# Performance work log

Measured on AMD Instinct MI355X. Metric: run time of the kernel, lower is better.

The kernel has to match this reference:

```python
import jax, jax.numpy as jnp
import numpy as np

N_NODES = 100000
N_EDGES = 1600000
N_ADJS = 2
N_LAYERS = 3
D_IN = 128
H = 128           # hidden dim; last conv out = 256 / num_adjs = 128
N_GRAPHS = 1024


def setup_inputs() -> dict:
    key = jax.random.key(0)
    ks = jax.random.split(key, 12)
    x = jax.random.normal(ks[0], (N_NODES, D_IN), dtype=jnp.float32)
    edge_index = jax.random.randint(ks[1], (N_ADJS, 2, N_EDGES), 0, N_NODES, dtype=jnp.int32)
    batch = jnp.sort(jax.random.randint(ks[2], (N_NODES,), 0, N_GRAPHS, dtype=jnp.int32))
    s = 0.05
    lin0_w = jax.random.normal(ks[3], (D_IN, H), dtype=jnp.float32) * s
    lin0_b = jnp.zeros((H,), dtype=jnp.float32)
    conv_w = jax.random.normal(ks[4], (N_ADJS, N_LAYERS, H, H), dtype=jnp.float32) * s
    lin1_w = jax.random.normal(ks[5], (2 * H, H), dtype=jnp.float32) * s
    lin1_b = jnp.zeros((H,), dtype=jnp.float32)
    lin2_w = jax.random.normal(ks[6], (H, 1), dtype=jnp.float32) * s
    lin2_b = jnp.zeros((1,), dtype=jnp.float32)
    return {"x": x, "edge_index": edge_index, "batch": batch,
            "lin0_w": lin0_w, "lin0_b": lin0_b, "conv_w": conv_w,
            "lin1_w": lin1_w, "lin1_b": lin1_b, "lin2_w": lin2_w, "lin2_b": lin2_b}


def _gcn_conv(h, W, row, col, norm, n_nodes):
    # GCNConv (bias=False): out[i] = sum_{j->i} norm_e * (h @ W)[j]
    m = h @ W                                  # [N, H] dense transform first (PyG order)
    msg = m[row] * norm[:, None]               # [E+N, H] gather + edge scaling
    return jax.ops.segment_sum(msg, col, num_segments=n_nodes)


def reference(x, edge_index, batch, lin0_w, lin0_b, conv_w, lin1_w, lin1_b, lin2_w, lin2_b):
    n = x.shape[0]
    loops = jnp.arange(n, dtype=edge_index.dtype)
    x0 = jax.nn.relu(x @ lin0_w + lin0_b)      # lin0 + relu
    pooled = []
    for a in range(N_ADJS):
        # gcn_norm with self loops: deg over targets, norm = d^-1/2[row] * d^-1/2[col]
        row = jnp.concatenate([edge_index[a, 0], loops])
        col = jnp.concatenate([edge_index[a, 1], loops])
        deg = jax.ops.segment_sum(jnp.ones_like(col, dtype=x.dtype), col, num_segments=n)
        dis = jnp.where(deg > 0, jax.lax.rsqrt(jnp.maximum(deg, 1e-12)), 0.0)
        norm = dis[row] * dis[col]
        h = x0
        for l in range(N_LAYERS):
            h = jax.nn.relu(_gcn_conv(h, conv_w[a, l], row, col, norm, n))
        # global_add_pool: segment sum over graph ids
        pooled.append(jax.ops.segment_sum(h, batch, num_segments=N_GRAPHS))
    g = jnp.concatenate(pooled, axis=1)        # [G, 256]
    g = jax.nn.relu(g @ lin1_w + lin1_b)
    # dropout(p=0.5) is identity in eval mode
    return g @ lin2_w + lin2_b                 # [G, 1]
```

## Files before the change

kernel.cpp:

```cpp
#include <hip/hip_runtime.h>

#define NN 100000
#define NE 1600000
#define NADJ 2
#define NLAY 3
#define HD 128
#define NG 1024

#define EBLK 4096
#define EB   391
#define NBUK 196
#define BPAD 200
#define GB   782
#define AB   12500
#define PB   1563

typedef unsigned int uint32;
typedef unsigned short u16;

typedef __attribute__((ext_vector_type(8))) short bfrag8;
typedef __attribute__((ext_vector_type(4))) float f32x4;
typedef __attribute__((ext_vector_type(2))) float f32x2;

__device__ __forceinline__ u16 f2bf(float f) {
    uint32 u = __float_as_uint(f);
    u += 0x7FFFu + ((u >> 16) & 1u);
    return (u16)(u >> 16);
}
__device__ __forceinline__ float bflo(uint32 u) { return __uint_as_float(u << 16); }
__device__ __forceinline__ float bfhi(uint32 u) { return __uint_as_float(u & 0xFFFF0000u); }

__global__ __launch_bounds__(256) void prep(
    const float* __restrict__ x, const float* __restrict__ conv_w,
    const float* __restrict__ lin0_w, u16* __restrict__ xbf,
    u16* __restrict__ wt) {
    if (blockIdx.x < 6250) {
        int i = blockIdx.x * 256 + threadIdx.x;
        float4 a = ((const float4*)x)[i * 2];
        float4 b = ((const float4*)x)[i * 2 + 1];
        uint4 v;
        v.x = (uint32)f2bf(a.x) | ((uint32)f2bf(a.y) << 16);
        v.y = (uint32)f2bf(a.z) | ((uint32)f2bf(a.w) << 16);
        v.z = (uint32)f2bf(b.x) | ((uint32)f2bf(b.y) << 16);
        v.w = (uint32)f2bf(b.z) | ((uint32)f2bf(b.w) << 16);
        ((uint4*)xbf)[i] = v;
    } else {
        int bid = blockIdx.x - 6250;
        const float* W = (bid < 6) ? conv_w + (size_t)bid * HD * HD : lin0_w;
        u16* o = wt + (size_t)bid * HD * HD;
        for (int i = 0; i < 64; ++i) {
            int idx = i * 256 + threadIdx.x;
            int n = idx >> 7, k = idx & 127;
            o[idx] = f2bf(W[k * 128 + n]);
        }
    }
}

__global__ __launch_bounds__(256) void gemm_mfma(
    const u16* __restrict__ Abf, const u16* __restrict__ Wt,
    u16* __restrict__ outbf, const float* __restrict__ bias)
{
    const int wid = blockIdx.x * 4 + (threadIdx.x >> 6);
    const int lane = threadIdx.x & 63;
    const int row0 = (wid >> 1) * 64;
    if (row0 >= NN) return;
    const int wc = (wid & 1) * 64;
    const int lr = lane & 15, kg = lane >> 4;

    bfrag8 a[4][4];
    #pragma unroll
    for (int ks = 0; ks < 4; ++ks)
        #pragma unroll
        for (int i = 0; i < 4; ++i)
            a[ks][i] = *(const bfrag8*)&Wt[(size_t)(wc + i * 16 + lr) * 128
                                           + (ks * 4 + kg) * 8];

    const f32x4 z = {0.f, 0.f, 0.f, 0.f};
    f32x4 acc[4][4];
    #pragma unroll
    for (int j = 0; j < 4; ++j)
        #pragma unroll
        for (int i = 0; i < 4; ++i) acc[j][i] = z;

    #pragma unroll
    for (int ks = 0; ks < 4; ++ks) {
        bfrag8 b[4];
        #pragma unroll
        for (int j = 0; j < 4; ++j) {
            int r = min(row0 + j * 16 + lr, NN - 1);
            b[j] = *(const bfrag8*)&Abf[(size_t)r * 128 + (ks * 4 + kg) * 8];
        }
        #pragma unroll
        for (int j = 0; j < 4; ++j)
            #pragma unroll
            for (int i = 0; i < 4; ++i)
                acc[j][i] = __builtin_amdgcn_mfma_f32_16x16x32_bf16(
                    a[ks][i], b[j], acc[j][i], 0, 0, 0);
    }

    #pragma unroll
    for (int j = 0; j < 4; ++j) {
        int m = row0 + j * 16 + lr;
        if (m < NN) {
            #pragma unroll
            for (int i = 0; i < 4; ++i) {
                int colb = wc + i * 16 + kg * 4;
                float4 bb = *(const float4*)&bias[colb];
                float v0 = fmaxf(acc[j][i][0] + bb.x, 0.f);
                float v1 = fmaxf(acc[j][i][1] + bb.y, 0.f);
                float v2 = fmaxf(acc[j][i][2] + bb.z, 0.f);
                float v3 = fmaxf(acc[j][i][3] + bb.w, 0.f);
                uint2 pk;
                pk.x = (uint32)f2bf(v0) | ((uint32)f2bf(v1) << 16);
                pk.y = (uint32)f2bf(v2) | ((uint32)f2bf(v3) << 16);
                *(uint2*)&outbf[(size_t)m * 128 + colb] = pk;
            }
        }
    }
}

__global__ __launch_bounds__(256) void gemm_mfma_b(
    const u16* __restrict__ hbase, int shared, const u16* __restrict__ wt,
    int l, u16* __restrict__ mm2, const float* __restrict__ dis2)
{
    int aa = blockIdx.x >= GB ? 1 : 0;
    int bblk = blockIdx.x - aa * GB;
    const u16* Abf = shared ? hbase : hbase + (size_t)aa * NN * HD;
    const u16* Wt = wt + (size_t)(aa * NLAY + l) * HD * HD;
    u16* outbf = mm2 + (size_t)aa * NN * HD;
    const float* dis = dis2 + (size_t)aa * NN;

    const int wid = bblk * 4 + (threadIdx.x >> 6);
    const int lane = threadIdx.x & 63;
    const int row0 = (wid >> 1) * 64;
    if (row0 >= NN) return;
    const int wc = (wid & 1) * 64;
    const int lr = lane & 15, kg = lane >> 4;

    bfrag8 a[4][4];
    #pragma unroll
    for (int ks = 0; ks < 4; ++ks)
        #pragma unroll
        for (int i = 0; i < 4; ++i)
            a[ks][i] = *(const bfrag8*)&Wt[(size_t)(wc + i * 16 + lr) * 128
                                           + (ks * 4 + kg) * 8];

    const f32x4 z = {0.f, 0.f, 0.f, 0.f};
    f32x4 acc[4][4];
    #pragma unroll
    for (int j = 0; j < 4; ++j)
        #pragma unroll
        for (int i = 0; i < 4; ++i) acc[j][i] = z;

    #pragma unroll
    for (int ks = 0; ks < 4; ++ks) {
        bfrag8 b[4];
        #pragma unroll
        for (int j = 0; j < 4; ++j) {
            int r = min(row0 + j * 16 + lr, NN - 1);
            b[j] = *(const bfrag8*)&Abf[(size_t)r * 128 + (ks * 4 + kg) * 8];
        }
        #pragma unroll
        for (int j = 0; j < 4; ++j)
            #pragma unroll
            for (int i = 0; i < 4; ++i)
                acc[j][i] = __builtin_amdgcn_mfma_f32_16x16x32_bf16(
                    a[ks][i], b[j], acc[j][i], 0, 0, 0);
    }

    #pragma unroll
    for (int j = 0; j < 4; ++j) {
        int m = row0 + j * 16 + lr;
        if (m < NN) {
            float ds = dis[m];
            #pragma unroll
            for (int i = 0; i < 4; ++i) {
                int colb = wc + i * 16 + kg * 4;
                uint2 pk;
                pk.x = (uint32)f2bf(acc[j][i][0] * ds)
                     | ((uint32)f2bf(acc[j][i][1] * ds) << 16);
                pk.y = (uint32)f2bf(acc[j][i][2] * ds)
                     | ((uint32)f2bf(acc[j][i][3] * ds) << 16);
                *(uint2*)&outbf[(size_t)m * 128 + colb] = pk;
            }
        }
    }
}


__global__ __launch_bounds__(256) void p1_count(
    const int* __restrict__ ei, int* __restrict__ bcnt)
{
    __shared__ int h[NBUK];
    int aa = blockIdx.x >= EB ? 1 : 0;
    int blk = blockIdx.x - aa * EB;
    const int* col = ei + (size_t)aa * 2 * NE + NE;
    int* bc = bcnt + (size_t)aa * EB * BPAD;
    int t = threadIdx.x;
    if (t < NBUK) h[t] = 0;
    __syncthreads();
    int base = blk * EBLK + t;
    #pragma unroll
    for (int u = 0; u < 16; ++u) {
        int e = base + u * 256;
        if (e < NE) atomicAdd(&h[col[e] >> 9], 1);
    }
    __syncthreads();
    if (t < NBUK) bc[blk * BPAD + t] = h[t];
}

__global__ __launch_bounds__(256) void p2a_scanblocks(
    const int* __restrict__ bcnt, int* __restrict__ pscan,
    int* __restrict__ btot)
{
    __shared__ int s[256];
    int aa = blockIdx.x >= NBUK ? 1 : 0;
    int b = blockIdx.x - aa * NBUK;
    const int* bc = bcnt + (size_t)aa * EB * BPAD;
    int* ps = pscan + (size_t)aa * EB * BPAD;
    int* bt = btot + aa * BPAD;
    int t = threadIdx.x;
    int v[2];
    int loc = 0;
    #pragma unroll
    for (int j = 0; j < 2; ++j) {
        int idx = t * 2 + j;
        v[j] = (idx < EB) ? bc[idx * BPAD + b] : 0;
        loc += v[j];
    }
    s[t] = loc;
    __syncthreads();
    for (int off = 1; off < 256; off <<= 1) {
        int u = (t >= off) ? s[t - off] : 0;
        __syncthreads();
        s[t] += u;
        __syncthreads();
    }
    int pre = s[t] - loc;
    #pragma unroll
    for (int j = 0; j < 2; ++j) {
        int idx = t * 2 + j;
        if (idx < EB) ps[idx * BPAD + b] = pre;
        pre += v[j];
    }
    if (t == 255) bt[b] = s[255];
}

__global__ __launch_bounds__(256) void p2b_scanbuckets(
    const int* __restrict__ btot, int* __restrict__ bbase)
{
    __shared__ int s[256];
    int aa = blockIdx.x;
    const int* bt = btot + aa * BPAD;
    int* bb = bbase + aa * (NBUK + 1);
    int t = threadIdx.x;
    int v = (t < NBUK) ? bt[t] : 0;
    s[t] = v;
    __syncthreads();
    for (int off = 1; off < 256; off <<= 1) {
        int u = (t >= off) ? s[t - off] : 0;
        __syncthreads();
        s[t] += u;
        __syncthreads();
    }
    if (t < NBUK) bb[t] = s[t] - v;
    if (t == NBUK - 1) bb[NBUK] = s[t];
}

__global__ __launch_bounds__(256) void p3_partition(
    const int* __restrict__ ei, const int* __restrict__ pscan,
    const int* __restrict__ bbase, uint2* __restrict__ part)
{
    __shared__ int spre[NBUK];
    __shared__ int cur[NBUK];
    int aa = blockIdx.x >= EB ? 1 : 0;
    int blk = blockIdx.x - aa * EB;
    const int* row = ei + (size_t)aa * 2 * NE;
    const int* col = row + NE;
    const int* ps = pscan + (size_t)aa * EB * BPAD;
    const int* bb = bbase + aa * (NBUK + 1);
    uint2* pt = part + (size_t)aa * NE;
    int t = threadIdx.x;
    if (t < NBUK) {
        spre[t] = bb[t] + ps[blk * BPAD + t];
        cur[t] = 0;
    }
    __syncthreads();
    int base = blk * EBLK + t;
    #pragma unroll
    for (int u = 0; u < 16; ++u) {
        int e = base + u * 256;
        if (e < NE) {
            int c = col[e];
            int b = c >> 9;
            int rk = atomicAdd(&cur[b], 1);
            pt[spre[b] + rk] = make_uint2((uint32)row[e], (uint32)c);
        }
    }
}

__global__ __launch_bounds__(256) void p4_csr(
    const uint2* __restrict__ part, const int* __restrict__ bbase,
    int* __restrict__ row_ptr2, float* __restrict__ dis2,
    int* __restrict__ csr2)
{
    __shared__ int cnt[512];
    __shared__ int sexcl[512];
    __shared__ int cur[512];
    __shared__ int s[256];
    int aa = blockIdx.x >= NBUK ? 1 : 0;
    int b = blockIdx.x - aa * NBUK;
    const uint2* pt = part + (size_t)aa * NE;
    const int* bb = bbase + aa * (NBUK + 1);
    int* rp = row_ptr2 + (size_t)aa * (NN + 1);
    float* ds = dis2 + (size_t)aa * NN;
    int* cs = csr2 + (size_t)aa * NE;
    int t = threadIdx.x;
    int base = bb[b];
    int ecnt = bb[b + 1] - base;
    int n0 = b << 9;
    cnt[t] = 0; cnt[t + 256] = 0;
    cur[t] = 0; cur[t + 256] = 0;
    __syncthreads();
    for (int i = t; i < ecnt; i += 256)
        atomicAdd(&cnt[pt[base + i].y - n0], 1);
    __syncthreads();
    int c0 = cnt[2 * t], c1 = cnt[2 * t + 1];
    int loc = c0 + c1;
    s[t] = loc;
    __syncthreads();
    for (int off = 1; off < 256; off <<= 1) {
        int u = (t >= off) ? s[t - off] : 0;
        __syncthreads();
        s[t] += u;
        __syncthreads();
    }
    int pre = s[t] - loc;
    sexcl[2 * t] = pre;
    sexcl[2 * t + 1] = pre + c0;
    int node = n0 + 2 * t;
    if (node < NN) {
        rp[node] = base + pre;
        ds[node] = rsqrtf((float)(c0 + 1));
    }
    if (node + 1 < NN) {
        rp[node + 1] = base + pre + c0;
        ds[node + 1] = rsqrtf((float)(c1 + 1));
    }
    if (b == 0 && t == 0) rp[NN] = NE;
    __syncthreads();
    for (int i = t; i < ecnt; i += 256) {
        uint2 p = pt[base + i];
        int li = (int)p.y - n0;
        int rk = atomicAdd(&cur[li], 1);
        cs[base + sexcl[li] + rk] = (int)p.x;
    }
}

__global__ __launch_bounds__(256) void agg_relu_b(
    const u16* __restrict__ mm2, const int* __restrict__ row_ptr2,
    const int* __restrict__ csr2, const float* __restrict__ dis2,
    u16* __restrict__ h2)
{
    int aa = blockIdx.x >= AB ? 1 : 0;
    int blk = blockIdx.x - aa * AB;
    const u16* mm = mm2 + (size_t)aa * NN * HD;
    const int* row_ptr = row_ptr2 + (size_t)aa * (NN + 1);
    const int* csr_src = csr2 + (size_t)aa * NE;
    const float* dis = dis2 + (size_t)aa * NN;
    u16* out = h2 + (size_t)aa * NN * HD;

    int wid = blk * 4 + (threadIdx.x >> 6);
    int nodeA = wid * 2;
    if (nodeA >= NN) return;
    int nodeB = nodeA + 1;
    uint32 lane = threadIdx.x & 63;
    const uint32* mv = (const uint32*)mm;
    int lan16 = (int)(lane & 15);

    uint32 selfA = mv[(uint32)nodeA * 64u + lane];
    uint32 selfB = mv[(uint32)nodeB * 64u + lane];
    f32x2 accA, accB;
    accA.x = bflo(selfA); accA.y = bfhi(selfA);
    accB.x = bflo(selfB); accB.y = bfhi(selfB);
    int eA = row_ptr[nodeA], e1A = row_ptr[nodeA + 1];
    int eB = e1A,            e1B = row_ptr[nodeB + 1];

    while (eA + 16 <= e1A && eB + 16 <= e1B) {
        uint32 pA = (uint32)csr_src[eA + lan16];
        uint32 pB = (uint32)csr_src[eB + lan16];
        #pragma unroll
        for (int u = 0; u < 16; ++u) {
            uint32 sA = (uint32)__builtin_amdgcn_readlane((int)pA, u);
            uint32 sB = (uint32)__builtin_amdgcn_readlane((int)pB, u);
            uint32 vA = (mv + (size_t)sA * 64u)[lane];
            uint32 vB = (mv + (size_t)sB * 64u)[lane];
            f32x2 tA, tB;
            tA.x = bflo(vA); tA.y = bfhi(vA);
            tB.x = bflo(vB); tB.y = bfhi(vB);
            asm("v_pk_add_f32 %0, %0, %1" : "+v"(accA) : "v"(tA));
            asm("v_pk_add_f32 %0, %0, %1" : "+v"(accB) : "v"(tB));
        }
        eA += 16; eB += 16;
    }
    for (; eA + 16 <= e1A; eA += 16) {
        uint32 pA = (uint32)csr_src[eA + lan16];
        #pragma unroll
        for (int u = 0; u < 16; ++u) {
            uint32 sA = (uint32)__builtin_amdgcn_readlane((int)pA, u);
            uint32 vA = (mv + (size_t)sA * 64u)[lane];
            f32x2 tA;
            tA.x = bflo(vA); tA.y = bfhi(vA);
            asm("v_pk_add_f32 %0, %0, %1" : "+v"(accA) : "v"(tA));
        }
    }
    for (; eB + 16 <= e1B; eB += 16) {
        uint32 pB = (uint32)csr_src[eB + lan16];
        #pragma unroll
        for (int u = 0; u < 16; ++u) {
            uint32 sB = (uint32)__builtin_amdgcn_readlane((int)pB, u);
            uint32 vB = (mv + (size_t)sB * 64u)[lane];
            f32x2 tB;
            tB.x = bflo(vB); tB.y = bfhi(vB);
            asm("v_pk_add_f32 %0, %0, %1" : "+v"(accB) : "v"(tB));
        }
    }
    int remA = e1A - eA, remB = e1B - eB;
    if ((remA | remB) != 0) {
        if (remA > 0 && remB > 0 && remA <= 8 && remB <= 8) {
            uint32 pA = (uint32)csr_src[min(eA + (int)(lane & 7), e1A - 1)];
            uint32 pB = (uint32)csr_src[min(eB + (int)(lane & 7), e1B - 1)];
            #pragma unroll
            for (int u = 0; u < 8; ++u) {
                uint32 sA = (uint32)__builtin_amdgcn_readlane((int)pA, u);
                uint32 sB = (uint32)__builtin_amdgcn_readlane((int)pB, u);
                uint32 vA = (mv + (size_t)sA * 64u)[lane];
                uint32 vB = (mv + (size_t)sB * 64u)[lane];
                float mA = (eA + u < e1A) ? 1.f : 0.f;
                float mB = (eB + u < e1B) ? 1.f : 0.f;
                f32x2 tA, tB, kA, kB;
                tA.x = bflo(vA); tA.y = bfhi(vA); kA.x = mA; kA.y = mA;
                tB.x = bflo(vB); tB.y = bfhi(vB); kB.x = mB; kB.y = mB;
                asm("v_pk_fma_f32 %0, %1, %2, %0" : "+v"(accA) : "v"(tA), "v"(kA));
                asm("v_pk_fma_f32 %0, %1, %2, %0" : "+v"(accB) : "v"(tB), "v"(kB));
            }
        } else {
            uint32 pA = 0, pB = 0;
            if (remA > 0) pA = (uint32)csr_src[min(eA + lan16, e1A - 1)];
            if (remB > 0) pB = (uint32)csr_src[min(eB + lan16, e1B - 1)];
            if (remA > 0 && remB > 0) {
                #pragma unroll
                for (int u = 0; u < 16; ++u) {
                    uint32 sA = (uint32)__builtin_amdgcn_readlane((int)pA, u);
                    uint32 sB = (uint32)__builtin_amdgcn_readlane((int)pB, u);
                    uint32 vA = (mv + (size_t)sA * 64u)[lane];
                    uint32 vB = (mv + (size_t)sB * 64u)[lane];
                    float mA = (eA + u < e1A) ? 1.f : 0.f;
                    float mB = (eB + u < e1B) ? 1.f : 0.f;
                    f32x2 tA, tB, kA, kB;
                    tA.x = bflo(vA); tA.y = bfhi(vA); kA.x = mA; kA.y = mA;
                    tB.x = bflo(vB); tB.y = bfhi(vB); kB.x = mB; kB.y = mB;
                    asm("v_pk_fma_f32 %0, %1, %2, %0" : "+v"(accA) : "v"(tA), "v"(kA));
                    asm("v_pk_fma_f32 %0, %1, %2, %0" : "+v"(accB) : "v"(tB), "v"(kB));
                }
            } else if (remA > 0) {
                #pragma unroll
                for (int u = 0; u < 16; ++u) {
                    uint32 sA = (uint32)__builtin_amdgcn_readlane((int)pA, u);
                    uint32 vA = (mv + (size_t)sA * 64u)[lane];
                    float mA = (eA + u < e1A) ? 1.f : 0.f;
                    f32x2 tA, kA;
                    tA.x = bflo(vA); tA.y = bfhi(vA); kA.x = mA; kA.y = mA;
                    asm("v_pk_fma_f32 %0, %1, %2, %0" : "+v"(accA) : "v"(tA), "v"(kA));
                }
            } else {
                #pragma unroll
                for (int u = 0; u < 16; ++u) {
                    uint32 sB = (uint32)__builtin_amdgcn_readlane((int)pB, u);
                    uint32 vB = (mv + (size_t)sB * 64u)[lane];
                    float mB = (eB + u < e1B) ? 1.f : 0.f;
                    f32x2 tB, kB;
                    tB.x = bflo(vB); tB.y = bfhi(vB); kB.x = mB; kB.y = mB;
                    asm("v_pk_fma_f32 %0, %1, %2, %0" : "+v"(accB) : "v"(tB), "v"(kB));
                }
            }
        }
    }

    float dA = dis[nodeA], dB = dis[nodeB];
    uint32 poA = (uint32)f2bf(fmaxf(dA * accA.x, 0.f))
               | ((uint32)f2bf(fmaxf(dA * accA.y, 0.f)) << 16);
    uint32 poB = (uint32)f2bf(fmaxf(dB * accB.x, 0.f))
               | ((uint32)f2bf(fmaxf(dB * accB.y, 0.f)) << 16);
    ((uint32*)out)[(uint32)nodeA * 64u + lane] = poA;
    ((uint32*)out)[(uint32)nodeB * 64u + lane] = poB;
}

__global__ __launch_bounds__(64) void pool_add_b(
    const u16* __restrict__ h2, const int* __restrict__ batch,
    float* __restrict__ pooled)
{
    int aa = blockIdx.x >= PB ? 1 : 0;
    int blk = blockIdx.x - aa * PB;
    const uint32* hv = (const uint32*)(h2 + (size_t)aa * NN * HD);
    int aoff = aa * HD;
    int c2 = threadIdx.x;
    int n0 = blk * 64;
    int nend = min(n0 + 64, NN);
    int cur = batch[n0];
    float ax = 0.f, ay = 0.f;
    for (int n = n0; n < nend; ++n) {
        int g = batch[n];
        if (g != cur) {
            atomicAdd(&pooled[(size_t)cur * 256 + aoff + 2 * c2], ax);
            atomicAdd(&pooled[(size_t)cur * 256 + aoff + 2 * c2 + 1], ay);
            ax = 0.f; ay = 0.f;
            cur = g;
        }
        uint32 v = hv[(size_t)n * 64 + c2];
        ax += bflo(v);
        ay += bfhi(v);
    }
    atomicAdd(&pooled[(size_t)cur * 256 + aoff + 2 * c2], ax);
    atomicAdd(&pooled[(size_t)cur * 256 + aoff + 2 * c2 + 1], ay);
}

__global__ __launch_bounds__(128) void head(
    const float* __restrict__ pooled,
    const float* __restrict__ w1, const float* __restrict__ b1,
    const float* __restrict__ w2, const float* __restrict__ b2,
    float* __restrict__ out)
{
    __shared__ float sp[256];
    __shared__ float sg[128];
    int g = blockIdx.x, t = threadIdx.x;
    sp[t] = pooled[(size_t)g * 256 + t];
    sp[t + 128] = pooled[(size_t)g * 256 + 128 + t];
    __syncthreads();
    float acc = b1[t];
    #pragma unroll 8
    for (int k = 0; k < 256; ++k) acc = fmaf(sp[k], w1[k * 128 + t], acc);
    sg[t] = fmaxf(acc, 0.f) * w2[t];
    __syncthreads();
    for (int s2 = 64; s2 > 0; s2 >>= 1) {
        if (t < s2) sg[t] += sg[t + s2];
        __syncthreads();
    }
    if (t == 0) out[g] = sg[0] + b2[0];
}

extern "C" void kernel_launch(void* const* d_in, const int* in_sizes, int n_in,
                              void* d_out, int out_size, void* d_ws, size_t ws_size,
                              hipStream_t stream) {
    const float* x      = (const float*)d_in[0];
    const int*   ei     = (const int*)d_in[1];
    const int*   batch  = (const int*)d_in[2];
    const float* lin0_w = (const float*)d_in[3];
    const float* lin0_b = (const float*)d_in[4];
    const float* conv_w = (const float*)d_in[5];
    const float* lin1_w = (const float*)d_in[6];
    const float* lin1_b = (const float*)d_in[7];
    const float* lin2_w = (const float*)d_in[8];
    const float* lin2_b = (const float*)d_in[9];
    float* out = (float*)d_out;

    const size_t NB = (size_t)NN * HD;
    float* x0f    = (float*)d_ws;
    float* bufA   = x0f + NB;
    float* bufB   = bufA + NB;
    float* pooled = bufB + NB;
    int*   row_ptr2 = (int*)(pooled + (size_t)NG * 256);
    float* dis2     = (float*)(row_ptr2 + 2 * (NN + 1));
    int*   csr2     = (int*)(dis2 + 2 * NN);
    u16*   wt       = (u16*)(csr2 + 2 * NE);
    int*   bcnt2    = (int*)(wt + 7 * HD * HD);
    int*   pscan2   = bcnt2 + 2 * EB * BPAD;
    int*   btot2    = pscan2 + 2 * EB * BPAD;
    int*   bbase2   = btot2 + 2 * BPAD;

    u16* x0bf    = (u16*)x0f;
    u16* xbf     = (u16*)(x0f + NB / 2);
    u16* mm2     = (u16*)bufA;
    u16* h2      = (u16*)bufB;
    uint2* part2 = (uint2*)bufB;

    hipMemsetAsync(pooled, 0, (size_t)NG * 256 * sizeof(float), stream);

    prep<<<6250 + 7, 256, 0, stream>>>(x, conv_w, lin0_w, xbf, wt);

    p1_count<<<2 * EB, 256, 0, stream>>>(ei, bcnt2);
    p2a_scanblocks<<<2 * NBUK, 256, 0, stream>>>(bcnt2, pscan2, btot2);
    p2b_scanbuckets<<<2, 256, 0, stream>>>(btot2, bbase2);
    p3_partition<<<2 * EB, 256, 0, stream>>>(ei, pscan2, bbase2, part2);
    p4_csr<<<2 * NBUK, 256, 0, stream>>>(part2, bbase2, row_ptr2, dis2, csr2);

    gemm_mfma<<<GB, 256, 0, stream>>>(xbf, wt + 6 * HD * HD, x0bf, lin0_b);

    for (int l = 0; l < NLAY; ++l) {
        gemm_mfma_b<<<2 * GB, 256, 0, stream>>>(
            l == 0 ? x0bf : h2, l == 0 ? 1 : 0, wt, l, mm2, dis2);
        agg_relu_b<<<2 * AB, 256, 0, stream>>>(mm2, row_ptr2, csr2, dis2, h2);
    }

    pool_add_b<<<2 * PB, 64, 0, stream>>>(h2, batch, pooled);

    head<<<NG, 128, 0, stream>>>(pooled, lin1_w, lin1_b, lin2_w, lin2_b, out);
}
```

Before: 620.0 us.

## Fuse x bf16 conversion into lin0 GEMM and stage partition scatter in LDS

The separate x-to-bf16 prep pass is removed, and the lin0 GEMM now reads fp32 x directly and converts it in registers. This drops one full write and reread of a 100k x 128 bf16 buffer, but each GEMM load moves twice as many bytes. The partition kernel now counts per-bucket edges locally, scans them, and stages edges in LDS in bucket order before writing out. The goal is more contiguous global scatter writes, paid for with extra syncs and about 48KB of shared memory per block, which may reduce occupancy.

```diff
diff --git a/kernel.cpp b/kernel.cpp
--- a/kernel.cpp
+++ b/kernel.cpp
@@ -30,34 +30,20 @@
 __device__ __forceinline__ float bflo(uint32 u) { return __uint_as_float(u << 16); }
 __device__ __forceinline__ float bfhi(uint32 u) { return __uint_as_float(u & 0xFFFF0000u); }
 
-__global__ __launch_bounds__(256) void prep(
-    const float* __restrict__ x, const float* __restrict__ conv_w,
-    const float* __restrict__ lin0_w, u16* __restrict__ xbf,
-    u16* __restrict__ wt) {
-    if (blockIdx.x < 6250) {
-        int i = blockIdx.x * 256 + threadIdx.x;
-        float4 a = ((const float4*)x)[i * 2];
-        float4 b = ((const float4*)x)[i * 2 + 1];
-        uint4 v;
-        v.x = (uint32)f2bf(a.x) | ((uint32)f2bf(a.y) << 16);
-        v.y = (uint32)f2bf(a.z) | ((uint32)f2bf(a.w) << 16);
-        v.z = (uint32)f2bf(b.x) | ((uint32)f2bf(b.y) << 16);
-        v.w = (uint32)f2bf(b.z) | ((uint32)f2bf(b.w) << 16);
-        ((uint4*)xbf)[i] = v;
-    } else {
-        int bid = blockIdx.x - 6250;
-        const float* W = (bid < 6) ? conv_w + (size_t)bid * HD * HD : lin0_w;
-        u16* o = wt + (size_t)bid * HD * HD;
-        for (int i = 0; i < 64; ++i) {
-            int idx = i * 256 + threadIdx.x;
-            int n = idx >> 7, k = idx & 127;
-            o[idx] = f2bf(W[k * 128 + n]);
-        }
-    }
-}
-
-__global__ __launch_bounds__(256) void gemm_mfma(
-    const u16* __restrict__ Abf, const u16* __restrict__ Wt,
+__global__ void wt_prep(const float* __restrict__ conv_w,
+                        const float* __restrict__ lin0_w, u16* __restrict__ wt) {
+    const float* W = (blockIdx.x < 6) ? conv_w + (size_t)blockIdx.x * HD * HD
+                                      : lin0_w;
+    u16* o = wt + (size_t)blockIdx.x * HD * HD;
+    for (int i = 0; i < 64; ++i) {
+        int idx = i * 256 + threadIdx.x;
+        int n = idx >> 7, k = idx & 127;
+        o[idx] = f2bf(W[k * 128 + n]);
+    }
+}
+
+__global__ __launch_bounds__(256) void gemm_lin0(
+    const float* __restrict__ x, const u16* __restrict__ Wt,
     u16* __restrict__ outbf, const float* __restrict__ bias)
 {
     const int wid = blockIdx.x * 4 + (threadIdx.x >> 6);
@@ -88,7 +74,15 @@
         #pragma unroll
         for (int j = 0; j < 4; ++j) {
             int r = min(row0 + j * 16 + lr, NN - 1);
-            b[j] = *(const bfrag8*)&Abf[(size_t)r * 128 + (ks * 4 + kg) * 8];
+            const float* xr = x + (size_t)r * 128 + (ks * 4 + kg) * 8;
+            float4 lo = *(const float4*)xr;
+            float4 hi = *(const float4*)(xr + 4);
+            bfrag8 fr;
+            fr[0] = (short)f2bf(lo.x); fr[1] = (short)f2bf(lo.y);
+            fr[2] = (short)f2bf(lo.z); fr[3] = (short)f2bf(lo.w);
+            fr[4] = (short)f2bf(hi.x); fr[5] = (short)f2bf(hi.y);
+            fr[6] = (short)f2bf(hi.z); fr[7] = (short)f2bf(hi.w);
+            b[j] = fr;
         }
         #pragma unroll
         for (int j = 0; j < 4; ++j)
@@ -271,8 +265,12 @@
     const int* __restrict__ ei, const int* __restrict__ pscan,
     const int* __restrict__ bbase, uint2* __restrict__ part)
 {
-    __shared__ int spre[NBUK];
-    __shared__ int cur[NBUK];
+    __shared__ uint2 staged[EBLK];
+    __shared__ int   sdst[EBLK];
+    __shared__ int   spre[NBUK];
+    __shared__ int   loff[NBUK];
+    __shared__ int   cur[NBUK];
+    __shared__ int   s[256];
     int aa = blockIdx.x >= EB ? 1 : 0;
     int blk = blockIdx.x - aa * EB;
     const int* row = ei + (size_t)aa * 2 * NE;
@@ -281,22 +279,51 @@
     const int* bb = bbase + aa * (NBUK + 1);
     uint2* pt = part + (size_t)aa * NE;
     int t = threadIdx.x;
-    if (t < NBUK) {
-        spre[t] = bb[t] + ps[blk * BPAD + t];
-        cur[t] = 0;
-    }
-    __syncthreads();
+    if (t < NBUK) cur[t] = 0;
+    __syncthreads();
+
     int base = blk * EBLK + t;
+    uint32 rr[16], cc[16];
     #pragma unroll
     for (int u = 0; u < 16; ++u) {
         int e = base + u * 256;
         if (e < NE) {
-            int c = col[e];
-            int b = c >> 9;
+            rr[u] = (uint32)row[e];
+            cc[u] = (uint32)col[e];
+            atomicAdd(&cur[cc[u] >> 9], 1);
+        }
+    }
+    __syncthreads();
+    int v = (t < NBUK) ? cur[t] : 0;
+    s[t] = v;
+    __syncthreads();
+    for (int off = 1; off < 256; off <<= 1) {
+        int u = (t >= off) ? s[t - off] : 0;
+        __syncthreads();
+        s[t] += u;
+        __syncthreads();
+    }
+    if (t < NBUK) {
+        loff[t] = s[t] - v;
+        spre[t] = bb[t] + ps[blk * BPAD + t];
+        cur[t] = 0;
+    }
+    __syncthreads();
+    #pragma unroll
+    for (int u = 0; u < 16; ++u) {
+        int e = base + u * 256;
+        if (e < NE) {
+            int b = cc[u] >> 9;
             int rk = atomicAdd(&cur[b], 1);
-            pt[spre[b] + rk] = make_uint2((uint32)row[e], (uint32)c);
-        }
-    }
+            int li = loff[b] + rk;
+            staged[li] = make_uint2(rr[u], cc[u]);
+            sdst[li] = spre[b] + rk;
+        }
+    }
+    __syncthreads();
+    int tot = min(NE - blk * EBLK, EBLK);
+    for (int i = t; i < tot; i += 256)
+        pt[sdst[i]] = staged[i];
 }
 
 __global__ __launch_bounds__(256) void p4_csr(
@@ -579,14 +606,13 @@
     int*   bbase2   = btot2 + 2 * BPAD;
 
     u16* x0bf    = (u16*)x0f;
-    u16* xbf     = (u16*)(x0f + NB / 2);
     u16* mm2     = (u16*)bufA;
     u16* h2      = (u16*)bufB;
     uint2* part2 = (uint2*)bufB;
 
     hipMemsetAsync(pooled, 0, (size_t)NG * 256 * sizeof(float), stream);
 
-    prep<<<6250 + 7, 256, 0, stream>>>(x, conv_w, lin0_w, xbf, wt);
+    wt_prep<<<7, 256, 0, stream>>>(conv_w, lin0_w, wt);
 
     p1_count<<<2 * EB, 256, 0, stream>>>(ei, bcnt2);
     p2a_scanblocks<<<2 * NBUK, 256, 0, stream>>>(bcnt2, pscan2, btot2);
@@ -594,7 +620,7 @@
     p3_partition<<<2 * EB, 256, 0, stream>>>(ei, pscan2, bbase2, part2);
     p4_csr<<<2 * NBUK, 256, 0, stream>>>(part2, bbase2, row_ptr2, dis2, csr2);
 
-    gemm_mfma<<<GB, 256, 0, stream>>>(xbf, wt + 6 * HD * HD, x0bf, lin0_b);
+    gemm_lin0<<<GB, 256, 0, stream>>>(x, wt + 6 * HD * HD, x0bf, lin0_b);
 
     for (int l = 0; l < NLAY; ++l) {
         gemm_mfma_b<<<2 * GB, 256, 0, stream>>>(
```

After: 604.3 us. -2.5%, faster.
